# Kernel optimization log

Measured on AMD Instinct MI355X. Metric: run time of the kernel, lower is better.

The kernel has to match this reference:

```python
import jax, jax.numpy as jnp
import numpy as np
import math

B, L, DIM, H = 1, 2048, 512, 8
D = DIM // H
STEPS = 1024
TWO_PI = 2.0 * math.pi
CHUNK = 64  # matches torch chunk_size


def setup_inputs() -> dict:
    key = jax.random.key(0)
    ks = jax.random.split(key, 6)
    x = jax.random.normal(ks[0], (B, L, DIM), jnp.float32)
    W_qs = jax.random.normal(ks[1], (DIM, 2 * DIM), jnp.float32) * 0.02
    b_qs = jnp.zeros((2 * DIM,), jnp.float32)
    ln_w = jnp.ones((2 * DIM,), jnp.float32)
    ln_b = jnp.zeros((2 * DIM,), jnp.float32)
    freq = jax.random.normal(ks[2], (H,), jnp.float32) * 0.02
    phase_shift = jax.random.normal(ks[3], (H,), jnp.float32) * 0.02
    W_out = jax.random.normal(ks[4], (DIM, DIM), jnp.float32) * 0.02
    b_out = jnp.zeros((DIM,), jnp.float32)
    # buffer: cos(linspace(0, 2pi, 1024)) exactly as in _init_lookup_tables
    cos_table = jnp.cos(jnp.linspace(0.0, TWO_PI, STEPS)).astype(jnp.float32)
    return dict(x=x, W_qs=W_qs, b_qs=b_qs, ln_w=ln_w, ln_b=ln_b,
                freq=freq, phase_shift=phase_shift, W_out=W_out, b_out=b_out,
                cos_table=cos_table)


def _forward(x, W_qs, b_qs, ln_w, ln_b, freq, phase_shift, W_out, b_out, cos_table):
    # quantum state preparation (shared module applied to same x => q == k states)
    qs = x @ W_qs + b_qs                                  # [B,L,2*DIM]
    mu = jnp.mean(qs, axis=-1, keepdims=True)
    var = jnp.var(qs, axis=-1, keepdims=True)
    qs = (qs - mu) / jnp.sqrt(var + 1e-5) * ln_w + ln_b    # LayerNorm(2*dim)
    amp, phase = jnp.split(qs, 2, axis=-1)                 # [B,L,DIM] each
    amp = jax.nn.sigmoid(amp)
    amp = amp / (jnp.sqrt(jnp.sum(amp ** 2, axis=-1, keepdims=True)) + 1e-8)
    phase = jnp.tanh(phase) * math.pi

    to_heads = lambda t: t.reshape(B, L, H, D).transpose(0, 2, 1, 3)  # [B,H,L,D]
    q_amp = to_heads(amp)
    q_phase = to_heads(phase)
    v = to_heads(x)

    NC = L // CHUNK
    qa_c = q_amp.reshape(B, H, NC, CHUNK, D).transpose(2, 0, 1, 3, 4)   # [NC,B,H,C,D]
    qp_c = q_phase.reshape(B, H, NC, CHUNK, D).transpose(2, 0, 1, 3, 4)
    f = freq[None, :, None, None, None]
    s = phase_shift[None, :, None, None, None]

    def chunk(carry, qc):
        qa, qp = qc                                         # [B,H,C,D]
        # pairwise per-dim phase interference via lookup table
        pd = (qp[:, :, :, None, :] - q_phase[:, :, None, :, :]) * f + s  # [B,H,C,L,D]
        idx = ((pd / TWO_PI * STEPS) % STEPS).astype(jnp.int32)
        interf = cos_table[idx]
        score = jnp.sum(qa[:, :, :, None, :] * q_amp[:, :, None, :, :] * interf,
                        axis=-1)                            # [B,H,C,L]
        return carry, score

    _, scores = jax.lax.scan(jax.checkpoint(chunk), 0, (qa_c, qp_c))
    scores = scores.transpose(1, 2, 0, 3, 4).reshape(B, H, L, L)
    attn = jax.nn.softmax(scores / math.sqrt(D), axis=-1)
    out = jnp.einsum('bhqk,bhkd->bhqd', attn, v)            # [B,H,L,D]
    out = out.transpose(0, 2, 1, 3).reshape(B, L, DIM)
    return out @ W_out + b_out


def reference(x, W_qs, b_qs, ln_w, ln_b, freq, phase_shift, W_out, b_out, cos_table):
    return _forward(x, W_qs, b_qs, ln_w, ln_b, freq, phase_shift, W_out, b_out, cos_table)
```

## Files before the change

### kernel.cpp

```cpp
#include <hip/hip_runtime.h>
#include <cstdint>
#include <cstddef>


typedef __attribute__((ext_vector_type(8))) short short8;
typedef __attribute__((ext_vector_type(4))) float f32x4;

#define MFMA16(a, b, c) __builtin_amdgcn_mfma_f32_16x16x32_bf16((a), (b), (c), 0, 0, 0)

static constexpr size_t B_ATTB = 0;
static constexpr size_t B_UB   = (size_t)2 * 1024 * 1024;
static constexpr size_t B_WB   = B_UB + (size_t)4 * 1024 * 1024;
static constexpr size_t B_VT   = B_WB + (size_t)4 * 1024 * 1024;
static constexpr size_t B_WQT  = B_VT + (size_t)2 * 1024 * 1024;
static constexpr size_t B_WOT  = B_WQT + (size_t)1 * 1024 * 1024;

__device__ __forceinline__ unsigned short f2bf(float f) {
  unsigned u = __float_as_uint(f);
  return (unsigned short)((u + 0x7FFFu + ((u >> 16) & 1u)) >> 16);
}

__device__ __forceinline__ void dma16(const unsigned short* g, unsigned char* l) {
  __builtin_amdgcn_global_load_lds((const unsigned int*)g, (unsigned int*)l,
                                   16, 0, 0);
}

__global__ __launch_bounds__(256) void k_prep(const float* __restrict__ x,
    const float* __restrict__ Wq, const float* __restrict__ Wo,
    unsigned short* __restrict__ vT, unsigned short* __restrict__ WqTp,
    unsigned short* __restrict__ WoT) {
  __shared__ float tl[64 * 65];
  const int t = threadIdx.x, b = blockIdx.x;
  if (b < 256) {
    const int i0 = (b >> 3) * 64, h = b & 7;
    #pragma unroll
    for (int it = 0; it < 16; ++it) {
      int n = t + 256 * it;
      int r = n >> 6, c = n & 63;
      tl[r * 65 + c] = x[(size_t)(i0 + r) * 512 + h * 64 + c];
    }
    __syncthreads();
    #pragma unroll
    for (int it = 0; it < 16; ++it) {
      int n = t + 256 * it;
      int d = n >> 6, ii = n & 63;
      vT[(size_t)(h * 64 + d) * 2048 + i0 + ii] = f2bf(tl[ii * 65 + d]);
    }
  } else if (b < 384) {
    const int bb = b - 256;
    const int k0 = (bb >> 4) * 64, n0 = (bb & 15) * 64;
    #pragma unroll
    for (int it = 0; it < 16; ++it) {
      int n = t + 256 * it;
      int r = n >> 6, c = n & 63;
      tl[r * 65 + c] = Wq[(size_t)(k0 + r) * 1024 + n0 + c];
    }
    __syncthreads();
    #pragma unroll
    for (int it = 0; it < 16; ++it) {
      int n = t + 256 * it;
      int rr = n >> 6, cc = n & 63;
      int nn = n0 + rr, kk = k0 + cc;
      int nt = nn >> 4, mm = nn & 15;
      int kc32 = kk >> 5, qd = (kk >> 3) & 3, j = kk & 7;
      WqTp[(((size_t)nt * 16 + kc32) * 64 + qd * 16 + mm) * 8 + j] =
          f2bf(tl[cc * 65 + rr]);
    }
  } else {
    const int bb = b - 384;
    const int k0 = (bb >> 3) * 64, n0 = (bb & 7) * 64;
    #pragma unroll
    for (int it = 0; it < 16; ++it) {
      int n = t + 256 * it;
      int r = n >> 6, c = n & 63;
      tl[r * 65 + c] = Wo[(size_t)(k0 + r) * 512 + n0 + c];
    }
    __syncthreads();
    #pragma unroll
    for (int it = 0; it < 16; ++it) {
      int n = t + 256 * it;
      int rr = n >> 6, cc = n & 63;
      WoT[(size_t)(n0 + rr) * 512 + k0 + cc] = f2bf(tl[cc * 65 + rr]);
    }
  }
}

__global__ __launch_bounds__(512, 2) void k_qs_ln(const float* __restrict__ x,
    const unsigned short* __restrict__ WqTp, const float* __restrict__ bq,
    const float* __restrict__ lnw, const float* __restrict__ lnb,
    const float* __restrict__ fr, const float* __restrict__ psh,
    unsigned short* __restrict__ Ub, unsigned short* __restrict__ Wb) {
  __shared__ __align__(16) unsigned char s_bb[2][65536];
  __shared__ __align__(16) unsigned short s_a[16 * 520];
  __shared__ float red[8 * 16 * 2];
  __shared__ float red2[4 * 16];
  float* s_amp = (float*)(&s_bb[0][0]);
  float* s_ph  = (float*)(&s_bb[1][0]);
  const int r0 = blockIdx.x * 16, t = threadIdx.x;
  const int w = t >> 6, lane = t & 63, m = lane & 15, quad = lane >> 4;
  const unsigned short* gB = WqTp + (size_t)w * 8192 + (size_t)lane * 8;
  #pragma unroll
  for (int it = 0; it < 8; ++it)
    dma16(gB + (size_t)it * 65536, s_bb[0] + (it * 8 + w) * 1024);
  {
    const int row = t >> 5, cs = (t & 31) * 16;
    const float4* xr = (const float4*)(x + (size_t)(r0 + row) * 512 + cs);
    unsigned short tmp[16];
    #pragma unroll
    for (int q4 = 0; q4 < 4; ++q4) {
      float4 v = xr[q4];
      tmp[q4 * 4 + 0] = f2bf(v.x); tmp[q4 * 4 + 1] = f2bf(v.y);
      tmp[q4 * 4 + 2] = f2bf(v.z); tmp[q4 * 4 + 3] = f2bf(v.w);
    }
    *(short8*)(s_a + row * 520 + cs)     = *(short8*)(tmp);
    *(short8*)(s_a + row * 520 + cs + 8) = *(short8*)(tmp + 8);
  }
  __syncthreads();
  f32x4 acc[8] = {{0,0,0,0},{0,0,0,0},{0,0,0,0},{0,0,0,0},
                  {0,0,0,0},{0,0,0,0},{0,0,0,0},{0,0,0,0}};
  for (int kc = 0; kc < 16; ++kc) {
    const int cur = kc & 1;
    if (kc < 15) {
      const unsigned short* g = gB + (size_t)(kc + 1) * 512;
      #pragma unroll
      for (int it = 0; it < 8; ++it)
        dma16(g + (size_t)it * 65536, s_bb[cur ^ 1] + (it * 8 + w) * 1024);
    }
    short8 af = *(const short8*)(s_a + m * 520 + kc * 32 + quad * 8);
    #pragma unroll
    for (int nt = 0; nt < 8; ++nt) {
      short8 bf = *(const short8*)(s_bb[cur] + (w * 8 + nt) * 1024 + lane * 16);
      acc[nt] = MFMA16(af, bf, acc[nt]);
    }
    __syncthreads();
  }
  #pragma unroll
  for (int nt = 0; nt < 8; ++nt) {
    float bv = bq[w * 128 + nt * 16 + m];
    #pragma unroll
    for (int r = 0; r < 4; ++r) acc[nt][r] += bv;
  }
  float s1[4] = {0, 0, 0, 0}, s2[4] = {0, 0, 0, 0};
  #pragma unroll
  for (int r = 0; r < 4; ++r)
    #pragma unroll
    for (int nt = 0; nt < 8; ++nt) {
      float v = acc[nt][r];
      s1[r] += v; s2[r] += v * v;
    }
  #pragma unroll
  for (int off = 1; off < 16; off <<= 1)
    #pragma unroll
    for (int r = 0; r < 4; ++r) {
      s1[r] += __shfl_xor(s1[r], off, 64);
      s2[r] += __shfl_xor(s2[r], off, 64);
    }
  if (m == 0)
    #pragma unroll
    for (int r = 0; r < 4; ++r) {
      red[(w * 16 + quad * 4 + r) * 2]     = s1[r];
      red[(w * 16 + quad * 4 + r) * 2 + 1] = s2[r];
    }
  __syncthreads();
  float mu[4], rstd[4];
  #pragma unroll
  for (int r = 0; r < 4; ++r) {
    int row = quad * 4 + r;
    float S = 0, S2 = 0;
    #pragma unroll
    for (int wp = 0; wp < 8; ++wp) {
      S  += red[(wp * 16 + row) * 2];
      S2 += red[(wp * 16 + row) * 2 + 1];
    }
    mu[r] = S * (1.0f / 1024.0f);
    float var = S2 * (1.0f / 1024.0f) - mu[r] * mu[r];
    rstd[r] = 1.0f / sqrtf(var + 1e-5f);
  }
  float y[8][4];
  #pragma unroll
  for (int nt = 0; nt < 8; ++nt) {
    int c = w * 128 + nt * 16 + m;
    float gw = lnw[c], gb = lnb[c];
    #pragma unroll
    for (int r = 0; r < 4; ++r)
      y[nt][r] = (acc[nt][r] - mu[r]) * rstd[r] * gw + gb;
  }
  const float PI_F = 3.14159265358979323846f;
  float a[8][4];
  if (w < 4) {
    float na[4] = {0, 0, 0, 0};
    #pragma unroll
    for (int nt = 0; nt < 8; ++nt)
      #pragma unroll
      for (int r = 0; r < 4; ++r) {
        float v = __builtin_amdgcn_rcpf(1.0f + __expf(-y[nt][r]));
        a[nt][r] = v;
        na[r] += v * v;
      }
    #pragma unroll
    for (int off = 1; off < 16; off <<= 1)
      #pragma unroll
      for (int r = 0; r < 4; ++r) na[r] += __shfl_xor(na[r], off, 64);
    if (m == 0)
      #pragma unroll
      for (int r = 0; r < 4; ++r) red2[w * 16 + quad * 4 + r] = na[r];
  } else {
    #pragma unroll
    for (int nt = 0; nt < 8; ++nt)
      #pragma unroll
      for (int r = 0; r < 4; ++r) {
        float e2 = __expf(2.0f * y[nt][r]);
        float p = (1.0f - 2.0f * __builtin_amdgcn_rcpf(e2 + 1.0f)) * PI_F;
        s_ph[(quad * 4 + r) * 516 + (w - 4) * 128 + nt * 16 + m] = p;
      }
  }
  __syncthreads();
  if (w < 4) {
    float inv[4];
    #pragma unroll
    for (int r = 0; r < 4; ++r) {
      int row = quad * 4 + r;
      float N = red2[row] + red2[16 + row] + red2[32 + row] + red2[48 + row];
      inv[r] = 1.0f / (sqrtf(N) + 1e-8f);
    }
    #pragma unroll
    for (int nt = 0; nt < 8; ++nt)
      #pragma unroll
      for (int r = 0; r < 4; ++r)
        s_amp[(quad * 4 + r) * 516 + w * 128 + nt * 16 + m] = a[nt][r] * inv[r];
  }
  __syncthreads();
  {
    const double GAM = 1024.0 / 1023.0;
    const int h  = lane >> 3;
    const int d0 = (lane & 7) * 8;
    const float c1  = (float)((double)fr[h]  * GAM);
    const float s1g = (float)((double)psh[h] * GAM);
    #pragma unroll
    for (int half = 0; half < 2; ++half) {
      const int row = half * 8 + w;
      const int i   = r0 + row;
      const float* ap = s_amp + row * 516 + h * 64 + d0;
      const float* pp = s_ph  + row * 516 + h * 64 + d0;
      short8 uc, us, wc, wsn;
      #pragma unroll
      for (int j = 0; j < 8; ++j) {
        float af = ap[j], p = pp[j];
        float A  = fmaf(p, c1, s1g);
        float Bp = p * c1;
        float cA, sA, cB, sB;
        __sincosf(A, &sA, &cA);
        __sincosf(Bp, &sB, &cB);
        uc[j]  = (short)f2bf(af * cA); us[j]  = (short)f2bf(af * sA);
        wc[j]  = (short)f2bf(af * cB); wsn[j] = (short)f2bf(af * sB);
      }
      size_t base = ((size_t)h * 2048 + i) * 128 + d0;
      *(short8*)(Ub + base)      = uc;
      *(short8*)(Ub + base + 64) = us;
      *(short8*)(Wb + base)      = wc;
      *(short8*)(Wb + base + 64) = wsn;
    }
  }
}

__global__ __launch_bounds__(512, 1) void k_flash6(const unsigned short* __restrict__ Ub,
    const unsigned short* __restrict__ Wb, const unsigned short* __restrict__ vT,
    unsigned short* __restrict__ attb) {
  __shared__ __align__(16) unsigned char s_w[2][128 * 272];
  __shared__ __align__(16) unsigned char s_v[2][64 * 272];
  __shared__ __align__(16) unsigned char s_p[2][64 * 272];
  const int qt = blockIdx.x, h = blockIdx.y;
  const int q0 = qt * 64;
  const int t = threadIdx.x;
  const int wave = t >> 6, lane = t & 63;
  const int qg = wave & 3, dh = wave >> 2;
  const int m = lane & 15, quad = lane >> 4;
  const int sr = t >> 2, sp = t & 3;
  const int vr = t >> 3, vp = t & 7;
  short8 afr[4][4];
  #pragma unroll
  for (int g = 0; g < 4; ++g) {
    const unsigned short* urow = Ub + ((size_t)h * 2048 + q0 + g * 16 + m) * 128;
    #pragma unroll
    for (int fs = 0; fs < 4; ++fs)
      afr[g][fs] = *(const short8*)(urow + fs * 32 + quad * 8);
  }
  short8 ones;
  #pragma unroll
  for (int j = 0; j < 8; ++j) ones[j] = (short)0x3F80;
  f32x4 oacc[2] = {{0,0,0,0},{0,0,0,0}};
  f32x4 dacc = {0, 0, 0, 0};
  const unsigned short* wgbase = Wb + (size_t)h * 2048 * 128 + (size_t)sr * 128;
  const unsigned short* vgbase = vT + ((size_t)h * 64 + vr) * 2048;
  #pragma unroll
  for (int it = 0; it < 4; ++it)
    *(short8*)(s_w[0] + sr * 272 + sp * 64 + it * 16) =
      *(const short8*)(wgbase + sp * 32 + it * 8);
  #pragma unroll
  for (int it = 0; it < 2; ++it)
    *(short8*)(s_v[0] + vr * 272 + vp * 32 + it * 16) =
      *(const short8*)(vgbase + vp * 16 + it * 8);
  __syncthreads();
  for (int kt = 0; kt < 16; ++kt) {
    const int cur = kt & 1;
    short8 wst[4], vst[2];
    const bool has = (kt < 15);
    if (has) {
      const unsigned short* wg = wgbase + (size_t)(kt + 1) * 128 * 128;
      #pragma unroll
      for (int it = 0; it < 4; ++it)
        wst[it] = *(const short8*)(wg + sp * 32 + it * 8);
      const unsigned short* vg = vgbase + (kt + 1) * 128;
      #pragma unroll
      for (int it = 0; it < 2; ++it)
        vst[it] = *(const short8*)(vg + vp * 16 + it * 8);
    }
    f32x4 sc[4] = {{0,0,0,0},{0,0,0,0},{0,0,0,0},{0,0,0,0}};
    #pragma unroll
    for (int fs = 0; fs < 4; ++fs) {
      short8 bfr = *(const short8*)(s_w[cur] + (wave * 16 + m) * 272 + fs * 64 + quad * 16);
      #pragma unroll
      for (int g = 0; g < 4; ++g)
        sc[g] = MFMA16(afr[g][fs], bfr, sc[g]);
    }
    #pragma unroll
    for (int g = 0; g < 4; ++g)
      #pragma unroll
      for (int r = 0; r < 4; ++r) {
        float p = __expf(sc[g][r] * 0.125f);
        *(unsigned short*)(s_p[cur] + (g * 16 + quad * 4 + r) * 272 +
                           (wave * 16 + m) * 2) = f2bf(p);
      }
    short8 vf[4][2];
    #pragma unroll
    for (int k2 = 0; k2 < 4; ++k2)
      #pragma unroll
      for (int dt = 0; dt < 2; ++dt)
        vf[k2][dt] = *(const short8*)(s_v[cur] + (dh * 32 + dt * 16 + m) * 272 +
                                      k2 * 64 + quad * 16);
    if (has) {
      #pragma unroll
      for (int it = 0; it < 4; ++it)
        *(short8*)(s_w[cur ^ 1] + sr * 272 + sp * 64 + it * 16) = wst[it];
      #pragma unroll
      for (int it = 0; it < 2; ++it)
        *(short8*)(s_v[cur ^ 1] + vr * 272 + vp * 32 + it * 16) = vst[it];
    }
    __syncthreads();
    #pragma unroll
    for (int k2 = 0; k2 < 4; ++k2) {
      short8 pf = *(const short8*)(s_p[cur] + (qg * 16 + m) * 272 + k2 * 64 + quad * 16);
      dacc = MFMA16(pf, ones, dacc);
      #pragma unroll
      for (int dt = 0; dt < 2; ++dt)
        oacc[dt] = MFMA16(pf, vf[k2][dt], oacc[dt]);
    }
  }
  float invd[4];
  #pragma unroll
  for (int r = 0; r < 4; ++r) invd[r] = 1.0f / dacc[r];
  #pragma unroll
  for (int dt = 0; dt < 2; ++dt)
    #pragma unroll
    for (int r = 0; r < 4; ++r)
      attb[(size_t)(q0 + qg * 16 + quad * 4 + r) * 512 + h * 64 +
           dh * 32 + dt * 16 + m] = f2bf(oacc[dt][r] * invd[r]);
}

__global__ __launch_bounds__(256) void k_gemm(const unsigned short* __restrict__ A,
    const unsigned short* __restrict__ Bt, const float* __restrict__ bias,
    float* __restrict__ C, int N) {
  __shared__ __align__(16) unsigned char sm[2 * 64 * 136];
  unsigned char* s_a = sm;
  unsigned char* s_b = sm + 64 * 136;
  const int m0 = blockIdx.x * 64, n0 = blockIdx.y * 64;
  const int t = threadIdx.x;
  const int wave = t >> 6, lane = t & 63;
  const int m = lane & 15, quad = lane >> 4;
  const int sr = t >> 2, spart = t & 3;
  f32x4 acc[4] = {{0,0,0,0},{0,0,0,0},{0,0,0,0},{0,0,0,0}};
  for (int kc = 0; kc < 512; kc += 64) {
    #pragma unroll
    for (int it = 0; it < 2; ++it) {
      *(short8*)(s_a + sr * 136 + spart * 32 + it * 16) =
        *(const short8*)(A + (size_t)(m0 + sr) * 512 + kc + spart * 16 + it * 8);
      *(short8*)(s_b + sr * 136 + spart * 32 + it * 16) =
        *(const short8*)(Bt + (size_t)(n0 + sr) * 512 + kc + spart * 16 + it * 8);
    }
    __syncthreads();
    #pragma unroll
    for (int k2 = 0; k2 < 2; ++k2) {
      short8 af = *(const short8*)(s_a + (wave * 16 + m) * 136 + k2 * 64 + quad * 16);
      #pragma unroll
      for (int nt = 0; nt < 4; ++nt) {
        short8 bf = *(const short8*)(s_b + (nt * 16 + m) * 136 + k2 * 64 + quad * 16);
        acc[nt] = MFMA16(af, bf, acc[nt]);
      }
    }
    __syncthreads();
  }
  #pragma unroll
  for (int nt = 0; nt < 4; ++nt) {
    int col = n0 + nt * 16 + m;
    float bv = bias[col];
    #pragma unroll
    for (int r = 0; r < 4; ++r) {
      int row = m0 + wave * 16 + quad * 4 + r;
      C[(size_t)row * N + col] = acc[nt][r] + bv;
    }
  }
}

extern "C" void kernel_launch(void* const* d_in, const int* in_sizes, int n_in,
                              void* d_out, int out_size, void* d_ws, size_t ws_size,
                              hipStream_t stream) {
  (void)in_sizes; (void)n_in; (void)out_size; (void)ws_size;
  const float* x   = (const float*)d_in[0];
  const float* Wq  = (const float*)d_in[1];
  const float* bq  = (const float*)d_in[2];
  const float* lnw = (const float*)d_in[3];
  const float* lnb = (const float*)d_in[4];
  const float* fr  = (const float*)d_in[5];
  const float* ps  = (const float*)d_in[6];
  const float* Wo  = (const float*)d_in[7];
  const float* bo  = (const float*)d_in[8];
  char* ws = (char*)d_ws;
  unsigned short* attb = (unsigned short*)(ws + B_ATTB);
  unsigned short* Ub   = (unsigned short*)(ws + B_UB);
  unsigned short* Wb   = (unsigned short*)(ws + B_WB);
  unsigned short* vT   = (unsigned short*)(ws + B_VT);
  unsigned short* WqTp = (unsigned short*)(ws + B_WQT);
  unsigned short* WoT  = (unsigned short*)(ws + B_WOT);
  float* out = (float*)d_out;

  k_prep<<<448, 256, 0, stream>>>(x, Wq, Wo, vT, WqTp, WoT);
  k_qs_ln<<<128, 512, 0, stream>>>(x, WqTp, bq, lnw, lnb, fr, ps, Ub, Wb);
  k_flash6<<<dim3(32, 8), 512, 0, stream>>>(Ub, Wb, vT, attb);
  k_gemm<<<dim3(32, 8), 256, 0, stream>>>(attb, WoT, bo, out, 512);
}
```

Before: 141.7 us.

## Fuse four kernels into one persistent kernel with software grid barriers

Merges the prep, projection+LayerNorm, flash attention and output GEMM kernels into a single 256-block persistent kernel separated by atomic-counter grid barriers. This removes three kernel launch gaps and their tail effects. Work is redistributed so each block handles two prep tiles and a halved-width GEMM tile. The risks are barrier spin overhead, idle blocks in the 128-block LN stage, and deadlock if the 256 blocks are not all co-resident.

Result: slower. 288.0 us (+103.2%).

```diff
diff --git a/kernel.cpp b/kernel.cpp
--- a/kernel.cpp
+++ b/kernel.cpp
@@ -25,388 +25,421 @@
                                    16, 0, 0);
 }
 
-__global__ __launch_bounds__(256) void k_prep(const float* __restrict__ x,
-    const float* __restrict__ Wq, const float* __restrict__ Wo,
-    unsigned short* __restrict__ vT, unsigned short* __restrict__ WqTp,
-    unsigned short* __restrict__ WoT) {
-  __shared__ float tl[64 * 65];
-  const int t = threadIdx.x, b = blockIdx.x;
-  if (b < 256) {
-    const int i0 = (b >> 3) * 64, h = b & 7;
-    #pragma unroll
-    for (int it = 0; it < 16; ++it) {
-      int n = t + 256 * it;
-      int r = n >> 6, c = n & 63;
-      tl[r * 65 + c] = x[(size_t)(i0 + r) * 512 + h * 64 + c];
-    }
-    __syncthreads();
-    #pragma unroll
-    for (int it = 0; it < 16; ++it) {
-      int n = t + 256 * it;
-      int d = n >> 6, ii = n & 63;
-      vT[(size_t)(h * 64 + d) * 2048 + i0 + ii] = f2bf(tl[ii * 65 + d]);
-    }
-  } else if (b < 384) {
-    const int bb = b - 256;
-    const int k0 = (bb >> 4) * 64, n0 = (bb & 15) * 64;
-    #pragma unroll
-    for (int it = 0; it < 16; ++it) {
-      int n = t + 256 * it;
-      int r = n >> 6, c = n & 63;
-      tl[r * 65 + c] = Wq[(size_t)(k0 + r) * 1024 + n0 + c];
-    }
-    __syncthreads();
-    #pragma unroll
-    for (int it = 0; it < 16; ++it) {
-      int n = t + 256 * it;
-      int rr = n >> 6, cc = n & 63;
-      int nn = n0 + rr, kk = k0 + cc;
-      int nt = nn >> 4, mm = nn & 15;
-      int kc32 = kk >> 5, qd = (kk >> 3) & 3, j = kk & 7;
-      WqTp[(((size_t)nt * 16 + kc32) * 64 + qd * 16 + mm) * 8 + j] =
-          f2bf(tl[cc * 65 + rr]);
-    }
-  } else {
-    const int bb = b - 384;
-    const int k0 = (bb >> 3) * 64, n0 = (bb & 7) * 64;
-    #pragma unroll
-    for (int it = 0; it < 16; ++it) {
-      int n = t + 256 * it;
-      int r = n >> 6, c = n & 63;
-      tl[r * 65 + c] = Wo[(size_t)(k0 + r) * 512 + n0 + c];
-    }
-    __syncthreads();
-    #pragma unroll
-    for (int it = 0; it < 16; ++it) {
-      int n = t + 256 * it;
-      int rr = n >> 6, cc = n & 63;
-      WoT[(size_t)(n0 + rr) * 512 + k0 + cc] = f2bf(tl[cc * 65 + rr]);
-    }
+__device__ unsigned g_bar[4];
+
+__device__ __forceinline__ void gridbar(int i) {
+  __syncthreads();
+  if (threadIdx.x == 0) {
+    __threadfence();
+    unsigned old = atomicAdd(&g_bar[i], 1u);
+    unsigned target = (old / 256u + 1u) * 256u;
+    while (__hip_atomic_load(&g_bar[i], __ATOMIC_ACQUIRE,
+                             __HIP_MEMORY_SCOPE_AGENT) < target)
+      __builtin_amdgcn_s_sleep(2);
+    __threadfence();
   }
+  __syncthreads();
 }
 
-__global__ __launch_bounds__(512, 2) void k_qs_ln(const float* __restrict__ x,
-    const unsigned short* __restrict__ WqTp, const float* __restrict__ bq,
+__global__ __launch_bounds__(512, 1) void k_fused(const float* __restrict__ x,
+    const float* __restrict__ Wq, const float* __restrict__ bq,
     const float* __restrict__ lnw, const float* __restrict__ lnb,
     const float* __restrict__ fr, const float* __restrict__ psh,
-    unsigned short* __restrict__ Ub, unsigned short* __restrict__ Wb) {
-  __shared__ __align__(16) unsigned char s_bb[2][65536];
-  __shared__ __align__(16) unsigned short s_a[16 * 520];
-  __shared__ float red[8 * 16 * 2];
-  __shared__ float red2[4 * 16];
-  float* s_amp = (float*)(&s_bb[0][0]);
-  float* s_ph  = (float*)(&s_bb[1][0]);
-  const int r0 = blockIdx.x * 16, t = threadIdx.x;
+    const float* __restrict__ Wo, const float* __restrict__ bo,
+    unsigned short* __restrict__ vT, unsigned short* __restrict__ WqTp,
+    unsigned short* __restrict__ WoT, unsigned short* __restrict__ Ub,
+    unsigned short* __restrict__ Wb, unsigned short* __restrict__ attb,
+    float* __restrict__ out) {
+  __shared__ __align__(16) unsigned char smem[148992];
+  const int t = threadIdx.x, b = blockIdx.x;
   const int w = t >> 6, lane = t & 63, m = lane & 15, quad = lane >> 4;
-  const unsigned short* gB = WqTp + (size_t)w * 8192 + (size_t)lane * 8;
-  #pragma unroll
-  for (int it = 0; it < 8; ++it)
-    dma16(gB + (size_t)it * 65536, s_bb[0] + (it * 8 + w) * 1024);
+
   {
-    const int row = t >> 5, cs = (t & 31) * 16;
-    const float4* xr = (const float4*)(x + (size_t)(r0 + row) * 512 + cs);
-    unsigned short tmp[16];
-    #pragma unroll
-    for (int q4 = 0; q4 < 4; ++q4) {
-      float4 v = xr[q4];
-      tmp[q4 * 4 + 0] = f2bf(v.x); tmp[q4 * 4 + 1] = f2bf(v.y);
-      tmp[q4 * 4 + 2] = f2bf(v.z); tmp[q4 * 4 + 3] = f2bf(v.w);
-    }
-    *(short8*)(s_a + row * 520 + cs)     = *(short8*)(tmp);
-    *(short8*)(s_a + row * 520 + cs + 8) = *(short8*)(tmp + 8);
+    const int ht = t >> 8, tt = t & 255;
+    const int u = ht ? (b + 256) : b;
+    const bool act = (ht == 0) || (b < 192);
+    float* tlh = (float*)(smem + ht * 16640);
+    if (act) {
+      if (u < 256) {
+        const int i0 = (u >> 3) * 64, h = u & 7;
+        #pragma unroll
+        for (int it = 0; it < 16; ++it) {
+          int n = tt + 256 * it;
+          int r = n >> 6, c = n & 63;
+          tlh[r * 65 + c] = x[(size_t)(i0 + r) * 512 + h * 64 + c];
+        }
+      } else if (u < 384) {
+        const int bb = u - 256;
+        const int k0 = (bb >> 4) * 64, n0 = (bb & 15) * 64;
+        #pragma unroll
+        for (int it = 0; it < 16; ++it) {
+          int n = tt + 256 * it;
+          int r = n >> 6, c = n & 63;
+          tlh[r * 65 + c] = Wq[(size_t)(k0 + r) * 1024 + n0 + c];
+        }
+      } else {
+        const int bb = u - 384;
+        const int k0 = (bb >> 3) * 64, n0 = (bb & 7) * 64;
+        #pragma unroll
+        for (int it = 0; it < 16; ++it) {
+          int n = tt + 256 * it;
+          int r = n >> 6, c = n & 63;
+          tlh[r * 65 + c] = Wo[(size_t)(k0 + r) * 512 + n0 + c];
+        }
+      }
+    }
+    __syncthreads();
+    if (act) {
+      if (u < 256) {
+        const int i0 = (u >> 3) * 64, h = u & 7;
+        #pragma unroll
+        for (int it = 0; it < 16; ++it) {
+          int n = tt + 256 * it;
+          int d = n >> 6, ii = n & 63;
+          vT[(size_t)(h * 64 + d) * 2048 + i0 + ii] = f2bf(tlh[ii * 65 + d]);
+        }
+      } else if (u < 384) {
+        const int bb = u - 256;
+        const int k0 = (bb >> 4) * 64, n0 = (bb & 15) * 64;
+        #pragma unroll
+        for (int it = 0; it < 16; ++it) {
+          int n = tt + 256 * it;
+          int rr = n >> 6, cc = n & 63;
+          int nn = n0 + rr, kk = k0 + cc;
+          int nt = nn >> 4, mm = nn & 15;
+          int kc32 = kk >> 5, qd = (kk >> 3) & 3, j = kk & 7;
+          WqTp[(((size_t)nt * 16 + kc32) * 64 + qd * 16 + mm) * 8 + j] =
+              f2bf(tlh[cc * 65 + rr]);
+        }
+      } else {
+        const int bb = u - 384;
+        const int k0 = (bb >> 3) * 64, n0 = (bb & 7) * 64;
+        #pragma unroll
+        for (int it = 0; it < 16; ++it) {
+          int n = tt + 256 * it;
+          int rr = n >> 6, cc = n & 63;
+          WoT[(size_t)(n0 + rr) * 512 + k0 + cc] = f2bf(tlh[cc * 65 + rr]);
+        }
+      }
+    }
   }
-  __syncthreads();
-  f32x4 acc[8] = {{0,0,0,0},{0,0,0,0},{0,0,0,0},{0,0,0,0},
-                  {0,0,0,0},{0,0,0,0},{0,0,0,0},{0,0,0,0}};
-  for (int kc = 0; kc < 16; ++kc) {
-    const int cur = kc & 1;
-    if (kc < 15) {
-      const unsigned short* g = gB + (size_t)(kc + 1) * 512;
-      #pragma unroll
-      for (int it = 0; it < 8; ++it)
-        dma16(g + (size_t)it * 65536, s_bb[cur ^ 1] + (it * 8 + w) * 1024);
-    }
-    short8 af = *(const short8*)(s_a + m * 520 + kc * 32 + quad * 8);
+  gridbar(0);
+
+  if (b < 128) {
+    float* s_amp = (float*)(smem);
+    float* s_ph  = (float*)(smem + 65536);
+    unsigned short* s_a = (unsigned short*)(smem + 131072);
+    float* red  = (float*)(smem + 147712);
+    float* red2 = (float*)(smem + 148736);
+    const int r0 = b * 16;
+    const unsigned short* gB = WqTp + (size_t)w * 8192 + (size_t)lane * 8;
+    #pragma unroll
+    for (int it = 0; it < 8; ++it)
+      dma16(gB + (size_t)it * 65536, smem + (it * 8 + w) * 1024);
+    {
+      const int row = t >> 5, cs = (t & 31) * 16;
+      const float4* xr = (const float4*)(x + (size_t)(r0 + row) * 512 + cs);
+      unsigned short tmp[16];
+      #pragma unroll
+      for (int q4 = 0; q4 < 4; ++q4) {
+        float4 v = xr[q4];
+        tmp[q4 * 4 + 0] = f2bf(v.x); tmp[q4 * 4 + 1] = f2bf(v.y);
+        tmp[q4 * 4 + 2] = f2bf(v.z); tmp[q4 * 4 + 3] = f2bf(v.w);
+      }
+      *(short8*)(s_a + row * 520 + cs)     = *(short8*)(tmp);
+      *(short8*)(s_a + row * 520 + cs + 8) = *(short8*)(tmp + 8);
+    }
+    __syncthreads();
+    f32x4 acc[8] = {{0,0,0,0},{0,0,0,0},{0,0,0,0},{0,0,0,0},
+                    {0,0,0,0},{0,0,0,0},{0,0,0,0},{0,0,0,0}};
+    for (int kc = 0; kc < 16; ++kc) {
+      const int cur = kc & 1;
+      if (kc < 15) {
+        const unsigned short* g = gB + (size_t)(kc + 1) * 512;
+        #pragma unroll
+        for (int it = 0; it < 8; ++it)
+          dma16(g + (size_t)it * 65536,
+                smem + (cur ^ 1) * 65536 + (it * 8 + w) * 1024);
+      }
+      short8 af = *(const short8*)(s_a + m * 520 + kc * 32 + quad * 8);
+      #pragma unroll
+      for (int nt = 0; nt < 8; ++nt) {
+        short8 bf = *(const short8*)(smem + cur * 65536 +
+                                     (w * 8 + nt) * 1024 + lane * 16);
+        acc[nt] = MFMA16(af, bf, acc[nt]);
+      }
+      __syncthreads();
+    }
     #pragma unroll
     for (int nt = 0; nt < 8; ++nt) {
-      short8 bf = *(const short8*)(s_bb[cur] + (w * 8 + nt) * 1024 + lane * 16);
-      acc[nt] = MFMA16(af, bf, acc[nt]);
-    }
-    __syncthreads();
-  }
-  #pragma unroll
-  for (int nt = 0; nt < 8; ++nt) {
-    float bv = bq[w * 128 + nt * 16 + m];
-    #pragma unroll
-    for (int r = 0; r < 4; ++r) acc[nt][r] += bv;
-  }
-  float s1[4] = {0, 0, 0, 0}, s2[4] = {0, 0, 0, 0};
-  #pragma unroll
-  for (int r = 0; r < 4; ++r)
-    #pragma unroll
-    for (int nt = 0; nt < 8; ++nt) {
-      float v = acc[nt][r];
-      s1[r] += v; s2[r] += v * v;
-    }
-  #pragma unroll
-  for (int off = 1; off < 16; off <<= 1)
-    #pragma unroll
-    for (int r = 0; r < 4; ++r) {
-      s1[r] += __shfl_xor(s1[r], off, 64);
-      s2[r] += __shfl_xor(s2[r], off, 64);
-    }
-  if (m == 0)
-    #pragma unroll
-    for (int r = 0; r < 4; ++r) {
-      red[(w * 16 + quad * 4 + r) * 2]     = s1[r];
-      red[(w * 16 + quad * 4 + r) * 2 + 1] = s2[r];
-    }
-  __syncthreads();
-  float mu[4], rstd[4];
-  #pragma unroll
-  for (int r = 0; r < 4; ++r) {
-    int row = quad * 4 + r;
-    float S = 0, S2 = 0;
-    #pragma unroll
-    for (int wp = 0; wp < 8; ++wp) {
-      S  += red[(wp * 16 + row) * 2];
-      S2 += red[(wp * 16 + row) * 2 + 1];
-    }
-    mu[r] = S * (1.0f / 1024.0f);
-    float var = S2 * (1.0f / 1024.0f) - mu[r] * mu[r];
-    rstd[r] = 1.0f / sqrtf(var + 1e-5f);
-  }
-  float y[8][4];
-  #pragma unroll
-  for (int nt = 0; nt < 8; ++nt) {
-    int c = w * 128 + nt * 16 + m;
-    float gw = lnw[c], gb = lnb[c];
+      float bv = bq[w * 128 + nt * 16 + m];
+      #pragma unroll
+      for (int r = 0; r < 4; ++r) acc[nt][r] += bv;
+    }
+    float s1[4] = {0, 0, 0, 0}, s2[4] = {0, 0, 0, 0};
     #pragma unroll
     for (int r = 0; r < 4; ++r)
-      y[nt][r] = (acc[nt][r] - mu[r]) * rstd[r] * gw + gb;
-  }
-  const float PI_F = 3.14159265358979323846f;
-  float a[8][4];
-  if (w < 4) {
-    float na[4] = {0, 0, 0, 0};
-    #pragma unroll
-    for (int nt = 0; nt < 8; ++nt)
+      #pragma unroll
+      for (int nt = 0; nt < 8; ++nt) {
+        float v = acc[nt][r];
+        s1[r] += v; s2[r] += v * v;
+      }
+    #pragma unroll
+    for (int off = 1; off < 16; off <<= 1)
       #pragma unroll
       for (int r = 0; r < 4; ++r) {
-        float v = __builtin_amdgcn_rcpf(1.0f + __expf(-y[nt][r]));
-        a[nt][r] = v;
-        na[r] += v * v;
-      }
-    #pragma unroll
-    for (int off = 1; off < 16; off <<= 1)
-      #pragma unroll
-      for (int r = 0; r < 4; ++r) na[r] += __shfl_xor(na[r], off, 64);
+        s1[r] += __shfl_xor(s1[r], off, 64);
+        s2[r] += __shfl_xor(s2[r], off, 64);
+      }
     if (m == 0)
       #pragma unroll
-      for (int r = 0; r < 4; ++r) red2[w * 16 + quad * 4 + r] = na[r];
-  } else {
-    #pragma unroll
-    for (int nt = 0; nt < 8; ++nt)
-      #pragma unroll
       for (int r = 0; r < 4; ++r) {
-        float e2 = __expf(2.0f * y[nt][r]);
-        float p = (1.0f - 2.0f * __builtin_amdgcn_rcpf(e2 + 1.0f)) * PI_F;
-        s_ph[(quad * 4 + r) * 516 + (w - 4) * 128 + nt * 16 + m] = p;
-      }
-  }
-  __syncthreads();
-  if (w < 4) {
-    float inv[4];
+        red[(w * 16 + quad * 4 + r) * 2]     = s1[r];
+        red[(w * 16 + quad * 4 + r) * 2 + 1] = s2[r];
+      }
+    __syncthreads();
+    float mu[4], rstd[4];
     #pragma unroll
     for (int r = 0; r < 4; ++r) {
       int row = quad * 4 + r;
-      float N = red2[row] + red2[16 + row] + red2[32 + row] + red2[48 + row];
-      inv[r] = 1.0f / (sqrtf(N) + 1e-8f);
-    }
-    #pragma unroll
-    for (int nt = 0; nt < 8; ++nt)
+      float S = 0, S2 = 0;
+      #pragma unroll
+      for (int wp = 0; wp < 8; ++wp) {
+        S  += red[(wp * 16 + row) * 2];
+        S2 += red[(wp * 16 + row) * 2 + 1];
+      }
+      mu[r] = S * (1.0f / 1024.0f);
+      float var = S2 * (1.0f / 1024.0f) - mu[r] * mu[r];
+      rstd[r] = 1.0f / sqrtf(var + 1e-5f);
+    }
+    float y[8][4];
+    #pragma unroll
+    for (int nt = 0; nt < 8; ++nt) {
+      int c = w * 128 + nt * 16 + m;
+      float gw = lnw[c], gb = lnb[c];
       #pragma unroll
       for (int r = 0; r < 4; ++r)
-        s_amp[(quad * 4 + r) * 516 + w * 128 + nt * 16 + m] = a[nt][r] * inv[r];
+        y[nt][r] = (acc[nt][r] - mu[r]) * rstd[r] * gw + gb;
+    }
+    const float PI_F = 3.14159265358979323846f;
+    float a[8][4];
+    if (w < 4) {
+      float na[4] = {0, 0, 0, 0};
+      #pragma unroll
+      for (int nt = 0; nt < 8; ++nt)
+        #pragma unroll
+        for (int r = 0; r < 4; ++r) {
+          float v = __builtin_amdgcn_rcpf(1.0f + __expf(-y[nt][r]));
+          a[nt][r] = v;
+          na[r] += v * v;
+        }
+      #pragma unroll
+      for (int off = 1; off < 16; off <<= 1)
+        #pragma unroll
+        for (int r = 0; r < 4; ++r) na[r] += __shfl_xor(na[r], off, 64);
+      if (m == 0)
+        #pragma unroll
+        for (int r = 0; r < 4; ++r) red2[w * 16 + quad * 4 + r] = na[r];
+    } else {
+      #pragma unroll
+      for (int nt = 0; nt < 8; ++nt)
+        #pragma unroll
+        for (int r = 0; r < 4; ++r) {
+          float e2 = __expf(2.0f * y[nt][r]);
+          float p = (1.0f - 2.0f * __builtin_amdgcn_rcpf(e2 + 1.0f)) * PI_F;
+          s_ph[(quad * 4 + r) * 516 + (w - 4) * 128 + nt * 16 + m] = p;
+        }
+    }
+    __syncthreads();
+    if (w < 4) {
+      float inv[4];
+      #pragma unroll
+      for (int r = 0; r < 4; ++r) {
+        int row = quad * 4 + r;
+        float N = red2[row] + red2[16 + row] + red2[32 + row] + red2[48 + row];
+        inv[r] = 1.0f / (sqrtf(N) + 1e-8f);
+      }
+      #pragma unroll
+      for (int nt = 0; nt < 8; ++nt)
+        #pragma unroll
+        for (int r = 0; r < 4; ++r)
+          s_amp[(quad * 4 + r) * 516 + w * 128 + nt * 16 + m] = a[nt][r] * inv[r];
+    }
+    __syncthreads();
+    {
+      const double GAM = 1024.0 / 1023.0;
+      const int h  = lane >> 3;
+      const int d0 = (lane & 7) * 8;
+      const float c1  = (float)((double)fr[h]  * GAM);
+      const float s1g = (float)((double)psh[h] * GAM);
+      #pragma unroll
+      for (int half = 0; half < 2; ++half) {
+        const int row = half * 8 + w;
+        const int i   = r0 + row;
+        const float* ap = s_amp + row * 516 + h * 64 + d0;
+        const float* pp = s_ph  + row * 516 + h * 64 + d0;
+        short8 uc, us, wc, wsn;
+        #pragma unroll
+        for (int j = 0; j < 8; ++j) {
+          float af = ap[j], p = pp[j];
+          float A  = fmaf(p, c1, s1g);
+          float Bp = p * c1;
+          float cA, sA, cB, sB;
+          __sincosf(A, &sA, &cA);
+          __sincosf(Bp, &sB, &cB);
+          uc[j]  = (short)f2bf(af * cA); us[j]  = (short)f2bf(af * sA);
+          wc[j]  = (short)f2bf(af * cB); wsn[j] = (short)f2bf(af * sB);
+        }
+        size_t base = ((size_t)h * 2048 + i) * 128 + d0;
+        *(short8*)(Ub + base)      = uc;
+        *(short8*)(Ub + base + 64) = us;
+        *(short8*)(Wb + base)      = wc;
+        *(short8*)(Wb + base + 64) = wsn;
+      }
+    }
   }
-  __syncthreads();
+  gridbar(1);
+
   {
-    const double GAM = 1024.0 / 1023.0;
-    const int h  = lane >> 3;
-    const int d0 = (lane & 7) * 8;
-    const float c1  = (float)((double)fr[h]  * GAM);
-    const float s1g = (float)((double)psh[h] * GAM);
-    #pragma unroll
-    for (int half = 0; half < 2; ++half) {
-      const int row = half * 8 + w;
-      const int i   = r0 + row;
-      const float* ap = s_amp + row * 516 + h * 64 + d0;
-      const float* pp = s_ph  + row * 516 + h * 64 + d0;
-      short8 uc, us, wc, wsn;
-      #pragma unroll
-      for (int j = 0; j < 8; ++j) {
-        float af = ap[j], p = pp[j];
-        float A  = fmaf(p, c1, s1g);
-        float Bp = p * c1;
-        float cA, sA, cB, sB;
-        __sincosf(A, &sA, &cA);
-        __sincosf(Bp, &sB, &cB);
-        uc[j]  = (short)f2bf(af * cA); us[j]  = (short)f2bf(af * sA);
-        wc[j]  = (short)f2bf(af * cB); wsn[j] = (short)f2bf(af * sB);
-      }
-      size_t base = ((size_t)h * 2048 + i) * 128 + d0;
-      *(short8*)(Ub + base)      = uc;
-      *(short8*)(Ub + base + 64) = us;
-      *(short8*)(Wb + base)      = wc;
-      *(short8*)(Wb + base + 64) = wsn;
-    }
+    unsigned char* sw0 = smem;
+    unsigned char* sv0 = smem + 69632;
+    unsigned char* sp0 = smem + 104448;
+    const int qt = b & 31, h = b >> 5;
+    const int q0 = qt * 64;
+    const int wave = w;
+    const int qg = wave & 3, dh = wave >> 2;
+    const int sr = t >> 2, sp = t & 3;
+    const int vr = t >> 3, vp = t & 7;
+    short8 afr[4][4];
+    #pragma unroll
+    for (int g = 0; g < 4; ++g) {
+      const unsigned short* urow = Ub + ((size_t)h * 2048 + q0 + g * 16 + m) * 128;
+      #pragma unroll
+      for (int fs = 0; fs < 4; ++fs)
+        afr[g][fs] = *(const short8*)(urow + fs * 32 + quad * 8);
+    }
+    short8 ones;
+    #pragma unroll
+    for (int j = 0; j < 8; ++j) ones[j] = (short)0x3F80;
+    f32x4 oacc[2] = {{0,0,0,0},{0,0,0,0}};
+    f32x4 dacc = {0, 0, 0, 0};
+    const unsigned short* wgbase = Wb + (size_t)h * 2048 * 128 + (size_t)sr * 128;
+    const unsigned short* vgbase = vT + ((size_t)h * 64 + vr) * 2048;
+    #pragma unroll
+    for (int it = 0; it < 4; ++it)
+      *(short8*)(sw0 + sr * 272 + sp * 64 + it * 16) =
+        *(const short8*)(wgbase + sp * 32 + it * 8);
+    #pragma unroll
+    for (int it = 0; it < 2; ++it)
+      *(short8*)(sv0 + vr * 272 + vp * 32 + it * 16) =
+        *(const short8*)(vgbase + vp * 16 + it * 8);
+    __syncthreads();
+    for (int kt = 0; kt < 16; ++kt) {
+      const int cur = kt & 1;
+      unsigned char* swc = sw0 + cur * 34816;
+      unsigned char* svc = sv0 + cur * 17408;
+      unsigned char* spc = sp0 + cur * 17408;
+      short8 wst[4], vst[2];
+      const bool has = (kt < 15);
+      if (has) {
+        const unsigned short* wg = wgbase + (size_t)(kt + 1) * 128 * 128;
+        #pragma unroll
+        for (int it = 0; it < 4; ++it)
+          wst[it] = *(const short8*)(wg + sp * 32 + it * 8);
+        const unsigned short* vg = vgbase + (kt + 1) * 128;
+        #pragma unroll
+        for (int it = 0; it < 2; ++it)
+          vst[it] = *(const short8*)(vg + vp * 16 + it * 8);
+      }
+      f32x4 sc[4] = {{0,0,0,0},{0,0,0,0},{0,0,0,0},{0,0,0,0}};
+      #pragma unroll
+      for (int fs = 0; fs < 4; ++fs) {
+        short8 bfr = *(const short8*)(swc + (wave * 16 + m) * 272 + fs * 64 + quad * 16);
+        #pragma unroll
+        for (int g = 0; g < 4; ++g)
+          sc[g] = MFMA16(afr[g][fs], bfr, sc[g]);
+      }
+      #pragma unroll
+      for (int g = 0; g < 4; ++g)
+        #pragma unroll
+        for (int r = 0; r < 4; ++r) {
+          float p = __expf(sc[g][r] * 0.125f);
+          *(unsigned short*)(spc + (g * 16 + quad * 4 + r) * 272 +
+                             (wave * 16 + m) * 2) = f2bf(p);
+        }
+      short8 vf[4][2];
+      #pragma unroll
+      for (int k2 = 0; k2 < 4; ++k2)
+        #pragma unroll
+        for (int dt = 0; dt < 2; ++dt)
+          vf[k2][dt] = *(const short8*)(svc + (dh * 32 + dt * 16 + m) * 272 +
+                                        k2 * 64 + quad * 16);
+      if (has) {
+        unsigned char* swn = sw0 + (cur ^ 1) * 34816;
+        unsigned char* svn = sv0 + (cur ^ 1) * 17408;
+        #pragma unroll
+        for (int it = 0; it < 4; ++it)
+          *(short8*)(swn + sr * 272 + sp * 64 + it * 16) = wst[it];
+        #pragma unroll
+        for (int it = 0; it < 2; ++it)
+          *(short8*)(svn + vr * 272 + vp * 32 + it * 16) = vst[it];
+      }
+      __syncthreads();
+      #pragma unroll
+      for (int k2 = 0; k2 < 4; ++k2) {
+        short8 pf = *(const short8*)(spc + (qg * 16 + m) * 272 + k2 * 64 + quad * 16);
+        dacc = MFMA16(pf, ones, dacc);
+        #pragma unroll
+        for (int dt = 0; dt < 2; ++dt)
+          oacc[dt] = MFMA16(pf, vf[k2][dt], oacc[dt]);
+      }
+    }
+    float invd[4];
+    #pragma unroll
+    for (int r = 0; r < 4; ++r) invd[r] = 1.0f / dacc[r];
+    #pragma unroll
+    for (int dt = 0; dt < 2; ++dt)
+      #pragma unroll
+      for (int r = 0; r < 4; ++r)
+        attb[(size_t)(q0 + qg * 16 + quad * 4 + r) * 512 + h * 64 +
+             dh * 32 + dt * 16 + m] = f2bf(oacc[dt][r] * invd[r]);
   }
-}
-
-__global__ __launch_bounds__(512, 1) void k_flash6(const unsigned short* __restrict__ Ub,
-    const unsigned short* __restrict__ Wb, const unsigned short* __restrict__ vT,
-    unsigned short* __restrict__ attb) {
-  __shared__ __align__(16) unsigned char s_w[2][128 * 272];
-  __shared__ __align__(16) unsigned char s_v[2][64 * 272];
-  __shared__ __align__(16) unsigned char s_p[2][64 * 272];
-  const int qt = blockIdx.x, h = blockIdx.y;
-  const int q0 = qt * 64;
-  const int t = threadIdx.x;
-  const int wave = t >> 6, lane = t & 63;
-  const int qg = wave & 3, dh = wave >> 2;
-  const int m = lane & 15, quad = lane >> 4;
-  const int sr = t >> 2, sp = t & 3;
-  const int vr = t >> 3, vp = t & 7;
-  short8 afr[4][4];
-  #pragma unroll
-  for (int g = 0; g < 4; ++g) {
-    const unsigned short* urow = Ub + ((size_t)h * 2048 + q0 + g * 16 + m) * 128;
-    #pragma unroll
-    for (int fs = 0; fs < 4; ++fs)
-      afr[g][fs] = *(const short8*)(urow + fs * 32 + quad * 8);
-  }
-  short8 ones;
-  #pragma unroll
-  for (int j = 0; j < 8; ++j) ones[j] = (short)0x3F80;
-  f32x4 oacc[2] = {{0,0,0,0},{0,0,0,0}};
-  f32x4 dacc = {0, 0, 0, 0};
-  const unsigned short* wgbase = Wb + (size_t)h * 2048 * 128 + (size_t)sr * 128;
-  const unsigned short* vgbase = vT + ((size_t)h * 64 + vr) * 2048;
-  #pragma unroll
-  for (int it = 0; it < 4; ++it)
-    *(short8*)(s_w[0] + sr * 272 + sp * 64 + it * 16) =
-      *(const short8*)(wgbase + sp * 32 + it * 8);
-  #pragma unroll
-  for (int it = 0; it < 2; ++it)
-    *(short8*)(s_v[0] + vr * 272 + vp * 32 + it * 16) =
-      *(const short8*)(vgbase + vp * 16 + it * 8);
-  __syncthreads();
-  for (int kt = 0; kt < 16; ++kt) {
-    const int cur = kt & 1;
-    short8 wst[4], vst[2];
-    const bool has = (kt < 15);
-    if (has) {
-      const unsigned short* wg = wgbase + (size_t)(kt + 1) * 128 * 128;
-      #pragma unroll
-      for (int it = 0; it < 4; ++it)
-        wst[it] = *(const short8*)(wg + sp * 32 + it * 8);
-      const unsigned short* vg = vgbase + (kt + 1) * 128;
-      #pragma unroll
-      for (int it = 0; it < 2; ++it)
-        vst[it] = *(const short8*)(vg + vp * 16 + it * 8);
-    }
-    f32x4 sc[4] = {{0,0,0,0},{0,0,0,0},{0,0,0,0},{0,0,0,0}};
-    #pragma unroll
-    for (int fs = 0; fs < 4; ++fs) {
-      short8 bfr = *(const short8*)(s_w[cur] + (wave * 16 + m) * 272 + fs * 64 + quad * 16);
-      #pragma unroll
-      for (int g = 0; g < 4; ++g)
-        sc[g] = MFMA16(afr[g][fs], bfr, sc[g]);
-    }
-    #pragma unroll
-    for (int g = 0; g < 4; ++g)
+  gridbar(2);
+
+  {
+    unsigned char* s_ga = smem;
+    unsigned char* s_gb = smem + 8704;
+    const int m0 = (b & 31) * 64, n0 = (b >> 5) * 64;
+    const int rw = w & 3, ch = w >> 2;
+    const int sr8 = t >> 3, sp8 = t & 7;
+    f32x4 acc2[2] = {{0,0,0,0},{0,0,0,0}};
+    for (int kc = 0; kc < 512; kc += 64) {
+      *(short8*)(s_ga + sr8 * 136 + sp8 * 16) =
+        *(const short8*)(attb + (size_t)(m0 + sr8) * 512 + kc + sp8 * 8);
+      *(short8*)(s_gb + sr8 * 136 + sp8 * 16) =
+        *(const short8*)(WoT + (size_t)(n0 + sr8) * 512 + kc + sp8 * 8);
+      __syncthreads();
+      #pragma unroll
+      for (int k2 = 0; k2 < 2; ++k2) {
+        short8 af = *(const short8*)(s_ga + (rw * 16 + m) * 136 + k2 * 64 + quad * 16);
+        #pragma unroll
+        for (int nt2 = 0; nt2 < 2; ++nt2) {
+          short8 bf = *(const short8*)(s_gb + ((ch * 2 + nt2) * 16 + m) * 136 +
+                                       k2 * 64 + quad * 16);
+          acc2[nt2] = MFMA16(af, bf, acc2[nt2]);
+        }
+      }
+      __syncthreads();
+    }
+    #pragma unroll
+    for (int nt2 = 0; nt2 < 2; ++nt2) {
+      int col = n0 + (ch * 2 + nt2) * 16 + m;
+      float bv = bo[col];
       #pragma unroll
       for (int r = 0; r < 4; ++r) {
-        float p = __expf(sc[g][r] * 0.125f);
-        *(unsigned short*)(s_p[cur] + (g * 16 + quad * 4 + r) * 272 +
-                           (wave * 16 + m) * 2) = f2bf(p);
-      }
-    short8 vf[4][2];
-    #pragma unroll
-    for (int k2 = 0; k2 < 4; ++k2)
-      #pragma unroll
-      for (int dt = 0; dt < 2; ++dt)
-        vf[k2][dt] = *(const short8*)(s_v[cur] + (dh * 32 + dt * 16 + m) * 272 +
-                                      k2 * 64 + quad * 16);
-    if (has) {
-      #pragma unroll
-      for (int it = 0; it < 4; ++it)
-        *(short8*)(s_w[cur ^ 1] + sr * 272 + sp * 64 + it * 16) = wst[it];
-      #pragma unroll
-      for (int it = 0; it < 2; ++it)
-        *(short8*)(s_v[cur ^ 1] + vr * 272 + vp * 32 + it * 16) = vst[it];
-    }
-    __syncthreads();
-    #pragma unroll
-    for (int k2 = 0; k2 < 4; ++k2) {
-      short8 pf = *(const short8*)(s_p[cur] + (qg * 16 + m) * 272 + k2 * 64 + quad * 16);
-      dacc = MFMA16(pf, ones, dacc);
-      #pragma unroll
-      for (int dt = 0; dt < 2; ++dt)
-        oacc[dt] = MFMA16(pf, vf[k2][dt], oacc[dt]);
-    }
-  }
-  float invd[4];
-  #pragma unroll
-  for (int r = 0; r < 4; ++r) invd[r] = 1.0f / dacc[r];
-  #pragma unroll
-  for (int dt = 0; dt < 2; ++dt)
-    #pragma unroll
-    for (int r = 0; r < 4; ++r)
-      attb[(size_t)(q0 + qg * 16 + quad * 4 + r) * 512 + h * 64 +
-           dh * 32 + dt * 16 + m] = f2bf(oacc[dt][r] * invd[r]);
-}
-
-__global__ __launch_bounds__(256) void k_gemm(const unsigned short* __restrict__ A,
-    const unsigned short* __restrict__ Bt, const float* __restrict__ bias,
-    float* __restrict__ C, int N) {
-  __shared__ __align__(16) unsigned char sm[2 * 64 * 136];
-  unsigned char* s_a = sm;
-  unsigned char* s_b = sm + 64 * 136;
-  const int m0 = blockIdx.x * 64, n0 = blockIdx.y * 64;
-  const int t = threadIdx.x;
-  const int wave = t >> 6, lane = t & 63;
-  const int m = lane & 15, quad = lane >> 4;
-  const int sr = t >> 2, spart = t & 3;
-  f32x4 acc[4] = {{0,0,0,0},{0,0,0,0},{0,0,0,0},{0,0,0,0}};
-  for (int kc = 0; kc < 512; kc += 64) {
-    #pragma unroll
-    for (int it = 0; it < 2; ++it) {
-      *(short8*)(s_a + sr * 136 + spart * 32 + it * 16) =
-        *(const short8*)(A + (size_t)(m0 + sr) * 512 + kc + spart * 16 + it * 8);
-      *(short8*)(s_b + sr * 136 + spart * 32 + it * 16) =
-        *(const short8*)(Bt + (size_t)(n0 + sr) * 512 + kc + spart * 16 + it * 8);
-    }
-    __syncthreads();
-    #pragma unroll
-    for (int k2 = 0; k2 < 2; ++k2) {
-      short8 af = *(const short8*)(s_a + (wave * 16 + m) * 136 + k2 * 64 + quad * 16);
-      #pragma unroll
-      for (int nt = 0; nt < 4; ++nt) {
-        short8 bf = *(const short8*)(s_b + (nt * 16 + m) * 136 + k2 * 64 + quad * 16);
-        acc[nt] = MFMA16(af, bf, acc[nt]);
-      }
-    }
-    __syncthreads();
-  }
-  #pragma unroll
-  for (int nt = 0; nt < 4; ++nt) {
-    int col = n0 + nt * 16 + m;
-    float bv = bias[col];
-    #pragma unroll
-    for (int r = 0; r < 4; ++r) {
-      int row = m0 + wave * 16 + quad * 4 + r;
-      C[(size_t)row * N + col] = acc[nt][r] + bv;
+        int row = m0 + rw * 16 + quad * 4 + r;
+        out[(size_t)row * 512 + col] = acc2[nt2][r] + bv;
+      }
     }
   }
 }
@@ -433,8 +466,6 @@
   unsigned short* WoT  = (unsigned short*)(ws + B_WOT);
   float* out = (float*)d_out;
 
-  k_prep<<<448, 256, 0, stream>>>(x, Wq, Wo, vT, WqTp, WoT);
-  k_qs_ln<<<128, 512, 0, stream>>>(x, WqTp, bq, lnw, lnb, fr, ps, Ub, Wb);
-  k_flash6<<<dim3(32, 8), 512, 0, stream>>>(Ub, Wb, vT, attb);
-  k_gemm<<<dim3(32, 8), 256, 0, stream>>>(attb, WoT, bo, out, 512);
+  k_fused<<<256, 512, 0, stream>>>(x, Wq, bq, lnw, lnb, fr, ps, Wo, bo,
+                                   vT, WqTp, WoT, Ub, Wb, attb, out);
 }
```
